# Kernel tuning notes

Hardware: AMD Instinct MI355X
Metric: run time of the kernel (lower is better)

## Reference

```python
import jax, jax.numpy as jnp
import numpy as np

N_WIRES = 9
N_QRAM_LAYERS = 3
N_QCLS_LAYERS = 5

X = jnp.array([[0, 1], [1, 0]], dtype=jnp.complex64)
CNOT = jnp.array([[1, 0, 0, 0], [0, 1, 0, 0], [0, 0, 0, 1], [0, 0, 1, 0]], dtype=jnp.complex64)


def _rx(t):
    c = jnp.cos(t / 2)
    s = jnp.sin(t / 2)
    # works for scalar t -> (2,2) or batched t [B] -> (B,2,2)
    return jnp.stack([jnp.stack([c + 0j, -1j * s], -1), jnp.stack([-1j * s, c + 0j], -1)], -2)


def _ry(t):
    c = jnp.cos(t / 2)
    s = jnp.sin(t / 2)
    return jnp.stack([jnp.stack([c, -s], -1), jnp.stack([s, c], -1)], -2).astype(jnp.complex64)


def _rz(t):
    e = jnp.exp(-0.5j * t)
    f = jnp.exp(0.5j * t)
    z = jnp.zeros_like(e)
    return jnp.stack([jnp.stack([e, z], -1), jnp.stack([z, f], -1)], -2)


def _rot(phi, theta, omega):
    # PennyLane Rot(phi, theta, omega) = RZ(omega) @ RY(theta) @ RZ(phi)
    return _rz(omega) @ _ry(theta) @ _rz(phi)


def _crz(t):
    e = jnp.exp(-0.5j * t)
    f = jnp.exp(0.5j * t)
    one = jnp.ones((), e.dtype)
    return jnp.diag(jnp.stack([one, one, e, f]))


def _crx(t):
    return jnp.eye(4, dtype=jnp.complex64).at[2:, 2:].set(_rx(t))


def apply_1q(state, U, w):
    # state: [B] + (2,)*N_WIRES ; wire w -> axis 1+w
    s = jnp.moveaxis(state, 1 + w, -1)
    if U.ndim == 3:  # per-sample gate (embedding)
        s = jnp.einsum('bij,b...j->b...i', U, s)
    else:
        s = jnp.einsum('ij,...j->...i', U, s)
    return jnp.moveaxis(s, -1, 1 + w)


def apply_2q(state, U, c, t):
    s = jnp.moveaxis(state, (1 + c, 1 + t), (-2, -1))
    shp = s.shape
    s = s.reshape(shp[:-2] + (4,))
    s = jnp.einsum('ij,...j->...i', U, s)
    return jnp.moveaxis(s.reshape(shp), (-2, -1), (1 + c, 1 + t))


def embed(state, adds):
    # AngleEmbedding: RX(adds[:, i]) on wire i
    for i in range(N_WIRES):
        state = apply_1q(state, _rx(adds[:, i]), i)
    return state


def entangle_block(state, p):
    # p: [36] = 4 params per wire-pair step
    j = 0
    for i in range(N_WIRES):
        ip = (i + 1) % N_WIRES
        state = apply_1q(state, _ry(p[j]), i)
        state = apply_1q(state, _ry(p[j + 1]), ip)
        state = apply_2q(state, CNOT, i, ip)
        state = apply_2q(state, _crz(p[j + 2]), i, ip)
        state = apply_1q(state, X, ip)
        state = apply_2q(state, _crx(p[j + 3]), i, ip)
        j += 4
    return state


def sel_layer(state, w, r):
    # one StronglyEntanglingLayers layer: Rot on each wire, then CNOT ring of range r
    for i in range(N_WIRES):
        state = apply_1q(state, _rot(w[i, 0], w[i, 1], w[i, 2]), i)
    for i in range(N_WIRES):
        state = apply_2q(state, CNOT, i, (i + r) % N_WIRES)
    return state


def circuit(adds, params, weights, params2):
    B = adds.shape[0]
    state = jnp.zeros((B,) + (2,) * N_WIRES, jnp.complex64)
    state = state.at[(slice(None),) + (0,) * N_WIRES].set(1.0)
    state = embed(state, adds)
    for l in range(N_QRAM_LAYERS):
        state = entangle_block(state, params[l * 36:(l + 1) * 36])
    for l in range(N_QRAM_LAYERS):
        r = (l % (N_WIRES - 1)) + 1  # PennyLane default ranges
        state = sel_layer(state, weights[l], r)
    for l in range(N_QCLS_LAYERS):
        state = entangle_block(state, params2[l * 36:(l + 1) * 36])
    probs = jnp.abs(state) ** 2
    p = probs.reshape(B, 2, -1).sum(-1)  # marginal over wire 0
    return p[:, 0] - p[:, 1]  # <PauliZ(0)>


def setup_inputs() -> dict:
    key = jax.random.key(0)
    k1, k2, k3, k4 = jax.random.split(key, 4)
    B = 8192
    return {
        'adds': jax.random.normal(k1, (B, N_WIRES), dtype=jnp.float32),
        'params': jax.random.normal(k2, (N_QRAM_LAYERS * 36,), dtype=jnp.float32),
        'weights': jax.random.normal(k3, (N_QRAM_LAYERS, N_WIRES, N_QRAM_LAYERS), dtype=jnp.float32),
        'params2': jax.random.normal(k4, (N_QCLS_LAYERS * 36,), dtype=jnp.float32),
    }


def reference(adds, params, weights, params2):
    return circuit(adds, params, weights, params2)
```

## Files before the change

kernel.cpp:

```cpp
#include <hip/hip_runtime.h>

#define NQ 9
#define NS 512
#define M2 1024

#define COEF_ROT_BASE (72*32)
#define COEF_FLOATS   (COEF_ROT_BASE + 27*8)

typedef __attribute__((ext_vector_type(8))) short bf16x8;
typedef __attribute__((ext_vector_type(4))) float f32x4;

__device__ inline unsigned short f2bf(float f){
  unsigned int u = __float_as_uint(f);
  u += 0x7fffu + ((u >> 16) & 1u);
  return (unsigned short)(u >> 16);
}


template<int LM>
__device__ inline float lxor(float v){
  if constexpr (LM == 1)
    return __int_as_float(__builtin_amdgcn_mov_dpp(__float_as_int(v), 0xB1, 0xF, 0xF, true));
  else if constexpr (LM == 2)
    return __int_as_float(__builtin_amdgcn_mov_dpp(__float_as_int(v), 0x4E, 0xF, 0xF, true));
  else if constexpr (LM == 3)
    return __int_as_float(__builtin_amdgcn_mov_dpp(__float_as_int(v), 0x1B, 0xF, 0xF, true));
  else if constexpr (LM < 32)
    return __int_as_float(__builtin_amdgcn_ds_swizzle(__float_as_int(v), (LM<<10)|0x1F));
  else
    return __shfl_xor(v, LM);
}

__device__ inline void apply_h(float& ax, float& ay, int p, const float* H,
                               float tx, float ty, float cx, float cy,
                               float bx, float by){
  const float* hx = H + p*4;
  const float* hy = H + 16 + p*4;
  float ox = ax, oy = ay;
  float nx = hx[0]*ox - hy[0]*oy + hx[1]*tx - hy[1]*ty
           + hx[2]*cx - hy[2]*cy + hx[3]*bx - hy[3]*by;
  float ny = hx[0]*oy + hy[0]*ox + hx[1]*ty + hy[1]*tx
           + hx[2]*cy + hy[2]*cx + hx[3]*by + hy[3]*bx;
  ax = nx; ay = ny;
}

template<int CM, int TM>
__device__ inline void step_lds(float& ax, float& ay, int i, float2* sh, const float* H){
  __syncthreads();
  sh[i] = make_float2(ax, ay);
  __syncthreads();
  float2 tv = sh[i ^ TM];
  float2 cv = sh[i ^ CM];
  float2 bv = sh[i ^ (CM ^ TM)];
  int p = ((i & CM) ? 2 : 0) | ((i & TM) ? 1 : 0);
  apply_h(ax, ay, p, H, tv.x, tv.y, cv.x, cv.y, bv.x, bv.y);
}

template<int CM, int TM>
__device__ inline void step_swz(float& ax, float& ay, int lane, const float* H){
  float tx = lxor<TM>(ax),      ty = lxor<TM>(ay);
  float cx = lxor<CM>(ax),      cy = lxor<CM>(ay);
  float bx = lxor<(CM^TM)>(ax), by = lxor<(CM^TM)>(ay);
  int p = ((lane & CM) ? 2 : 0) | ((lane & TM) ? 1 : 0);
  apply_h(ax, ay, p, H, tx, ty, cx, cy, bx, by);
}

template<int PM>
__device__ inline void rot_lds(float& ax, float& ay, int i, float2* sh, const float* U){
  __syncthreads();
  sh[i] = make_float2(ax, ay);
  __syncthreads();
  float2 pv = sh[i ^ PM];
  const float* u = U + (((i & PM) ? 1 : 0) << 2);
  float nx = u[0]*ax - u[1]*ay + u[2]*pv.x - u[3]*pv.y;
  float ny = u[0]*ay + u[1]*ax + u[2]*pv.y + u[3]*pv.x;
  ax = nx; ay = ny;
}

template<int LM>
__device__ inline void rot_swz(float& ax, float& ay, int lane, const float* U){
  float px = lxor<LM>(ax), py = lxor<LM>(ay);
  const float* u = U + (((lane & LM) ? 1 : 0) << 2);
  float nx = u[0]*ax - u[1]*ay + u[2]*px - u[3]*py;
  float ny = u[0]*ay + u[1]*ax + u[2]*py + u[3]*px;
  ax = nx; ay = ny;
}

__device__ inline void ring_rt(float& ax, float& ay, int i, float2* sh, int R){
  __syncthreads();
  sh[i] = make_float2(ax, ay);
  __syncthreads();
  int s = i;
  for (int k = 8; k >= 0; --k){
    int bc = 8 - k;
    int it = k + R; if (it >= 9) it -= 9;
    int bt = 8 - it;
    s ^= ((s >> bc) & 1) << bt;
  }
  float2 v = sh[s];
  ax = v.x; ay = v.y;
}


template<int I = 0>
__device__ inline void ent_blk(float& ax, float& ay, int i, int lane, float2* sh,
                               const float* Gbase){
  const float* H = Gbase + I*32;
  if constexpr      (I == 0) step_lds<0x100,0x080>(ax, ay, i, sh, H);
  else if constexpr (I == 1) step_lds<0x080,0x040>(ax, ay, i, sh, H);
  else if constexpr (I == 2) step_lds<0x040,0x020>(ax, ay, i, sh, H);
  else if constexpr (I == 3) step_swz<0x20,0x10>(ax, ay, lane, H);
  else if constexpr (I == 4) step_swz<0x10,0x08>(ax, ay, lane, H);
  else if constexpr (I == 5) step_swz<0x08,0x04>(ax, ay, lane, H);
  else if constexpr (I == 6) step_swz<0x04,0x02>(ax, ay, lane, H);
  else if constexpr (I == 7) step_swz<0x02,0x01>(ax, ay, lane, H);
  else                       step_lds<0x001,0x100>(ax, ay, i, sh, H);
  if constexpr (I < 8) ent_blk<I+1>(ax, ay, i, lane, sh, Gbase);
}

template<int I = 0>
__device__ inline void sel_rots_rt(float& ax, float& ay, int i, int lane, float2* sh,
                                   const float* ubase){
  const float* u = ubase + I*8;
  if constexpr      (I == 0) rot_lds<0x100>(ax, ay, i, sh, u);
  else if constexpr (I == 1) rot_lds<0x080>(ax, ay, i, sh, u);
  else if constexpr (I == 2) rot_lds<0x040>(ax, ay, i, sh, u);
  else if constexpr (I == 3) rot_swz<0x20>(ax, ay, lane, u);
  else if constexpr (I == 4) rot_swz<0x10>(ax, ay, lane, u);
  else if constexpr (I == 5) rot_swz<0x08>(ax, ay, lane, u);
  else if constexpr (I == 6) rot_swz<0x04>(ax, ay, lane, u);
  else if constexpr (I == 7) rot_swz<0x02>(ax, ay, lane, u);
  else                       rot_swz<0x01>(ax, ay, lane, u);
  if constexpr (I < 8) sel_rots_rt<I+1>(ax, ay, i, lane, sh, ubase);
}

__global__ __launch_bounds__(512) void sim_V(const float* __restrict__ params,
                                             const float* __restrict__ weights,
                                             const float* __restrict__ params2,
                                             unsigned short* __restrict__ A2){
  __shared__ float2 sh[512];
  __shared__ float scoef[COEF_FLOATS];
  int tid = threadIdx.x;

  if (tid < 72){
    int blk = tid / 9, I = tid % 9;
    const float* p = (blk < 3) ? params + blk*36 : params2 + (blk-3)*36;
    float s0,c0,s1,c1,s2,c2,s3,c3;
    __sincosf(0.5f*p[4*I+0], &s0, &c0);
    __sincosf(0.5f*p[4*I+1], &s1, &c1);
    __sincosf(0.5f*p[4*I+2], &s2, &c2);
    __sincosf(0.5f*p[4*I+3], &s3, &c3);
    float m[4][4] = {
      { c0*c1, -c0*s1, -s0*c1,  s0*s1},
      { c0*s1,  c0*c1, -s0*s1, -s0*c1},
      { s0*c1, -s0*s1,  c0*c1, -c0*s1},
      { s0*s1,  s0*c1,  c0*s1,  c0*c1}};
    float gx[4][4], gy[4][4];
    #pragma unroll
    for (int q = 0; q < 4; ++q){
      gx[0][q] = m[1][q];  gy[0][q] = 0.f;
      gx[1][q] = m[0][q];  gy[1][q] = 0.f;
      gx[2][q] =  c3*c2*m[2][q] - s3*s2*m[3][q];
      gy[2][q] =  c3*s2*m[2][q] - s3*c2*m[3][q];
      gx[3][q] =  s3*s2*m[2][q] + c3*c2*m[3][q];
      gy[3][q] = -(s3*c2*m[2][q] + c3*s2*m[3][q]);
    }
    float* dst = scoef + tid*32;
    #pragma unroll
    for (int pp = 0; pp < 4; ++pp)
      #pragma unroll
      for (int d = 0; d < 4; ++d){
        dst[pp*4+d]    = gx[pp][pp^d];
        dst[16+pp*4+d] = gy[pp][pp^d];
      }
  } else if (tid < 99){
    int r = tid - 72;
    int l = r / 9, i = r % 9;
    const float* w = weights + l*27 + 3*i;
    float phi = w[0], th = w[1], om = w[2];
    float sT,cT,sA,cA,sB,cB;
    __sincosf(0.5f*th, &sT, &cT);
    __sincosf(0.5f*(phi+om), &sA, &cA);
    __sincosf(0.5f*(om-phi), &sB, &cB);
    float* dst = scoef + COEF_ROT_BASE + r*8;
    dst[0] =  cA*cT;  dst[1] = -sA*cT;
    dst[2] = -cB*sT;  dst[3] =  sB*sT;
    dst[4] =  cA*cT;  dst[5] =  sA*cT;
    dst[6] =  cB*sT;  dst[7] =  sB*sT;
  }
  __syncthreads();

  int t = blockIdx.x;
  int i = tid;
  int lane = tid & 63;
  float ax, ay;
  int pc = __popc((unsigned)t) & 3;
  float prx = (pc==0) ? 1.f : (pc==2 ? -1.f : 0.f);
  float pry = (pc==3) ? 1.f : (pc==1 ? -1.f : 0.f);
  ax = (i == t) ? prx : 0.f;
  ay = (i == t) ? pry : 0.f;

  #pragma unroll 1
  for (int blk = 0; blk < 3; ++blk)
    ent_blk<0>(ax, ay, i, lane, sh, scoef + blk*288);
  #pragma unroll 1
  for (int L = 0; L < 3; ++L){
    sel_rots_rt<0>(ax, ay, i, lane, sh, scoef + COEF_ROT_BASE + L*72);
    ring_rt(ax, ay, i, sh, L + 1);
  }
  #pragma unroll 1
  for (int blk = 3; blk < 8; ++blk)
    ent_blk<0>(ax, ay, i, lane, sh, scoef + blk*288);

  A2[(size_t)i * NS + t]        = f2bf(ax);
  A2[(size_t)(i + NS) * NS + t] = f2bf(ay);
}

__global__ __launch_bounds__(256) void prep(const float* __restrict__ adds,
                                            unsigned short* __restrict__ cT,
                                            float* __restrict__ out, int B){
  int gid = blockIdx.x * 256 + threadIdx.x;
  int b = gid >> 6;
  int lane = gid & 63;
  if (b < B){
    const float* ab = adds + b * NQ;
    float cw[NQ], sw[NQ];
    #pragma unroll
    for (int w = 0; w < NQ; ++w)
      __sincosf(0.5f * ab[w], &sw[w], &cw[w]);
    float p6 = 1.f;
    #pragma unroll
    for (int w = 0; w < 6; ++w)
      p6 *= ((lane >> (5 - w)) & 1) ? sw[w] : cw[w];
    union { unsigned short u[8]; uint4 v; } pk;
    #pragma unroll
    for (int j = 0; j < 8; ++j){
      float p = p6 * (((j>>2)&1) ? sw[6] : cw[6])
                   * (((j>>1)&1) ? sw[7] : cw[7])
                   * (( j    &1) ? sw[8] : cw[8]);
      pk.u[j] = f2bf(p);
    }
    *(uint4*)(cT + (size_t)b * NS + lane*8) = pk.v;
  }
  if (gid < B) out[gid] = 0.f;
}

__global__ __launch_bounds__(256) void gemm_out(const unsigned short* __restrict__ A2,
                                                const unsigned short* __restrict__ cT,
                                                float* __restrict__ out){
  int bx = blockIdx.x;
  int by = blockIdx.y;
  int tid = threadIdx.x;
  int wave = tid >> 6, lane = tid & 63;
  int wy = wave >> 1, wx = wave & 1;
  int lane15 = lane & 15, quad = lane >> 4;
  int rowBase = by*128 + wy*64;
  int colBase = bx*128 + wx*64;
  const short* Ap = (const short*)A2;
  const short* Bp = (const short*)cT;

  f32x4 acc[4][4];
  #pragma unroll
  for (int i = 0; i < 4; ++i)
    #pragma unroll
    for (int j = 0; j < 4; ++j)
      acc[i][j] = (f32x4){0.f, 0.f, 0.f, 0.f};

  #pragma unroll 2
  for (int k0 = 0; k0 < NS; k0 += 32){
    bf16x8 a[4], b[4];
    #pragma unroll
    for (int mi = 0; mi < 4; ++mi)
      a[mi] = *(const bf16x8*)(Ap + (size_t)(rowBase + mi*16 + lane15)*NS + k0 + quad*8);
    #pragma unroll
    for (int ni = 0; ni < 4; ++ni)
      b[ni] = *(const bf16x8*)(Bp + (size_t)(colBase + ni*16 + lane15)*NS + k0 + quad*8);
    #pragma unroll
    for (int mi = 0; mi < 4; ++mi)
      #pragma unroll
      for (int ni = 0; ni < 4; ++ni)
        acc[mi][ni] = __builtin_amdgcn_mfma_f32_16x16x32_bf16(a[mi], b[ni], acc[mi][ni], 0, 0, 0);
  }

  float sign = (by & 2) ? -1.f : 1.f;
  #pragma unroll
  for (int ni = 0; ni < 4; ++ni){
    float cs = 0.f;
    #pragma unroll
    for (int mi = 0; mi < 4; ++mi)
      #pragma unroll
      for (int r = 0; r < 4; ++r)
        cs += acc[mi][ni][r] * acc[mi][ni][r];
    cs += __shfl_xor(cs, 16);
    cs += __shfl_xor(cs, 32);
    if (quad == 0)
      atomicAdd(out + colBase + ni*16 + lane15, sign * cs);
  }
}

extern "C" void kernel_launch(void* const* d_in, const int* in_sizes, int n_in,
                              void* d_out, int out_size, void* d_ws, size_t ws_size,
                              hipStream_t stream) {
  const float* adds    = (const float*)d_in[0];
  const float* params  = (const float*)d_in[1];
  const float* weights = (const float*)d_in[2];
  const float* params2 = (const float*)d_in[3];
  float* out = (float*)d_out;
  int B = in_sizes[0] / NQ;

  unsigned short* A2 = (unsigned short*)d_ws;
  unsigned short* cT = A2 + (size_t)M2 * NS;

  hipLaunchKernelGGL(sim_V, dim3(NS), dim3(512), 0, stream, params, weights, params2, A2);
  hipLaunchKernelGGL(prep, dim3((B * 64 + 255) / 256), dim3(256), 0, stream, adds, cT, out, B);
  hipLaunchKernelGGL(gemm_out, dim3(B / 128, 8), dim3(256), 0, stream, A2, cT, out);
}
```

Before: 119.9 us.

## Precompute gate coefficients once, fuse prep into sim kernel, factor in-wave gates

Gate coefficient computation moves out of each of the 512 sim blocks into a single-block precoef kernel that writes to workspace, so the per-block sincos work and its barrier go away. The prep (embedding) work is merged into the simulation kernel as extra blocks so the two run in one launch. In-wave entangling steps are rewritten as three sequential factored rotations using DPP/swizzle instead of a dense 4x4 complex matrix, which cuts arithmetic. Coefficients are now read from global memory rather than LDS, and the extra launch adds a dependency.

```diff
diff --git a/kernel.cpp b/kernel.cpp
--- a/kernel.cpp
+++ b/kernel.cpp
@@ -14,6 +14,68 @@
   unsigned int u = __float_as_uint(f);
   u += 0x7fffu + ((u >> 16) & 1u);
   return (unsigned short)(u >> 16);
+}
+
+__global__ __launch_bounds__(128) void precoef(const float* __restrict__ params,
+                                               const float* __restrict__ weights,
+                                               const float* __restrict__ params2,
+                                               float* __restrict__ coef){
+  int tid = threadIdx.x;
+  if (tid < 72){
+    int blk = tid / 9, I = tid % 9;
+    const float* p = (blk < 3) ? params + blk*36 : params2 + (blk-3)*36;
+    float s0,c0,s1,c1,s2,c2,s3,c3;
+    __sincosf(0.5f*p[4*I+0], &s0, &c0);
+    __sincosf(0.5f*p[4*I+1], &s1, &c1);
+    __sincosf(0.5f*p[4*I+2], &s2, &c2);
+    __sincosf(0.5f*p[4*I+3], &s3, &c3);
+    float* dst = coef + tid*32;
+    if (I == 0 || I == 1 || I == 2 || I == 8){
+      float m[4][4] = {
+        { c0*c1, -c0*s1, -s0*c1,  s0*s1},
+        { c0*s1,  c0*c1, -s0*s1, -s0*c1},
+        { s0*c1, -s0*s1,  c0*c1, -c0*s1},
+        { s0*s1,  s0*c1,  c0*s1,  c0*c1}};
+      float gx[4][4], gy[4][4];
+      #pragma unroll
+      for (int q = 0; q < 4; ++q){
+        gx[0][q] = m[1][q];  gy[0][q] = 0.f;
+        gx[1][q] = m[0][q];  gy[1][q] = 0.f;
+        gx[2][q] =  c3*c2*m[2][q] - s3*s2*m[3][q];
+        gy[2][q] =  c3*s2*m[2][q] - s3*c2*m[3][q];
+        gx[3][q] =  s3*s2*m[2][q] + c3*c2*m[3][q];
+        gy[3][q] = -(s3*c2*m[2][q] + c3*s2*m[3][q]);
+      }
+      #pragma unroll
+      for (int pp = 0; pp < 4; ++pp)
+        #pragma unroll
+        for (int d = 0; d < 4; ++d){
+          dst[pp*4+d]    = gx[pp][pp^d];
+          dst[16+pp*4+d] = gy[pp][pp^d];
+        }
+    } else {
+      dst[0] = c0;  dst[1] = s0;
+      dst[2] = c1;  dst[3] = s1;
+      dst[4] =  c3*c2;  dst[5] =  c3*s2;
+      dst[6] = -s3*s2;  dst[7] = -s3*c2;
+      #pragma unroll
+      for (int k = 8; k < 32; ++k) dst[k] = 0.f;
+    }
+  } else if (tid < 99){
+    int r = tid - 72;
+    int l = r / 9, i = r % 9;
+    const float* w = weights + l*27 + 3*i;
+    float phi = w[0], th = w[1], om = w[2];
+    float sT,cT,sA,cA,sB,cB;
+    __sincosf(0.5f*th, &sT, &cT);
+    __sincosf(0.5f*(phi+om), &sA, &cA);
+    __sincosf(0.5f*(om-phi), &sB, &cB);
+    float* dst = coef + COEF_ROT_BASE + r*8;
+    dst[0] =  cA*cT;  dst[1] = -sA*cT;
+    dst[2] = -cB*sT;  dst[3] =  sB*sT;
+    dst[4] =  cA*cT;  dst[5] =  sA*cT;
+    dst[6] =  cB*sT;  dst[7] =  sB*sT;
+  }
 }
 
 
@@ -31,58 +93,77 @@
     return __shfl_xor(v, LM);
 }
 
-__device__ inline void apply_h(float& ax, float& ay, int p, const float* H,
-                               float tx, float ty, float cx, float cy,
-                               float bx, float by){
-  const float* hx = H + p*4;
-  const float* hy = H + 16 + p*4;
-  float ox = ax, oy = ay;
-  float nx = hx[0]*ox - hy[0]*oy + hx[1]*tx - hy[1]*ty
-           + hx[2]*cx - hy[2]*cy + hx[3]*bx - hy[3]*by;
-  float ny = hx[0]*oy + hy[0]*ox + hx[1]*ty + hy[1]*tx
-           + hx[2]*cy + hy[2]*cx + hx[3]*by + hy[3]*bx;
-  ax = nx; ay = ny;
-}
-
 template<int CM, int TM>
-__device__ inline void step_lds(float& ax, float& ay, int i, float2* sh, const float* H){
+__device__ inline void step_h(float& ax, float& ay, int i, float2* sh,
+                              const float* __restrict__ g){
   __syncthreads();
   sh[i] = make_float2(ax, ay);
   __syncthreads();
   float2 tv = sh[i ^ TM];
   float2 cv = sh[i ^ CM];
   float2 bv = sh[i ^ (CM ^ TM)];
-  int p = ((i & CM) ? 2 : 0) | ((i & TM) ? 1 : 0);
-  apply_h(ax, ay, p, H, tv.x, tv.y, cv.x, cv.y, bv.x, bv.y);
+  bool cb = (i & CM) != 0, tb = (i & TM) != 0;
+  float hx[4], hy[4];
+  #pragma unroll
+  for (int d = 0; d < 4; ++d){
+    hx[d] = cb ? (tb ? g[12+d] : g[8+d]) : (tb ? g[4+d] : g[d]);
+    hy[d] = cb ? (tb ? g[28+d] : g[24+d]) : (tb ? g[20+d] : g[16+d]);
+  }
+  float ox = ax, oy = ay;
+  ax = hx[0]*ox - hy[0]*oy + hx[1]*tv.x - hy[1]*tv.y
+     + hx[2]*cv.x - hy[2]*cv.y + hx[3]*bv.x - hy[3]*bv.y;
+  ay = hx[0]*oy + hy[0]*ox + hx[1]*tv.y + hy[1]*tv.x
+     + hx[2]*cv.y + hy[2]*cv.x + hx[3]*bv.y + hy[3]*bv.x;
 }
 
 template<int CM, int TM>
-__device__ inline void step_swz(float& ax, float& ay, int lane, const float* H){
-  float tx = lxor<TM>(ax),      ty = lxor<TM>(ay);
-  float cx = lxor<CM>(ax),      cy = lxor<CM>(ay);
-  float bx = lxor<(CM^TM)>(ax), by = lxor<(CM^TM)>(ay);
-  int p = ((lane & CM) ? 2 : 0) | ((lane & TM) ? 1 : 0);
-  apply_h(ax, ay, p, H, tx, ty, cx, cy, bx, by);
+__device__ inline void step_3r(float& ax, float& ay, int lane,
+                               const float* __restrict__ g){
+  float c0=g[0], s0=g[1], c1=g[2], s1=g[3];
+  float Ax=g[4], Ay=g[5], Bx=g[6], By=g[7];
+  {
+    float px = lxor<CM>(ax), py = lxor<CM>(ay);
+    float se = (lane & CM) ? s0 : -s0;
+    ax = c0*ax + se*px;  ay = c0*ay + se*py;
+  }
+  {
+    float px = lxor<TM>(ax), py = lxor<TM>(ay);
+    float se = (lane & TM) ? s1 : -s1;
+    ax = c1*ax + se*px;  ay = c1*ay + se*py;
+  }
+  {
+    float px = lxor<TM>(ax), py = lxor<TM>(ay);
+    bool tb = (lane & TM) != 0;
+    float Ay2 = tb ? -Ay : Ay, Bx2 = tb ? -Bx : Bx;
+    float nx = Ax*ax - Ay2*ay + Bx2*px - By*py;
+    float ny = Ax*ay + Ay2*ax + Bx2*py + By*px;
+    bool cb = (lane & CM) != 0;
+    ax = cb ? nx : px;  ay = cb ? ny : py;
+  }
 }
 
 template<int PM>
-__device__ inline void rot_lds(float& ax, float& ay, int i, float2* sh, const float* U){
+__device__ inline void rot_img(float& ax, float& ay, int i, float2* sh,
+                               const float* __restrict__ u){
   __syncthreads();
   sh[i] = make_float2(ax, ay);
   __syncthreads();
   float2 pv = sh[i ^ PM];
-  const float* u = U + (((i & PM) ? 1 : 0) << 2);
-  float nx = u[0]*ax - u[1]*ay + u[2]*pv.x - u[3]*pv.y;
-  float ny = u[0]*ay + u[1]*ax + u[2]*pv.y + u[3]*pv.x;
+  bool hi = (i & PM) != 0;
+  float u0 = hi?u[4]:u[0], u1 = hi?u[5]:u[1], u2 = hi?u[6]:u[2], u3 = hi?u[7]:u[3];
+  float nx = u0*ax - u1*ay + u2*pv.x - u3*pv.y;
+  float ny = u0*ay + u1*ax + u2*pv.y + u3*pv.x;
   ax = nx; ay = ny;
 }
 
 template<int LM>
-__device__ inline void rot_swz(float& ax, float& ay, int lane, const float* U){
+__device__ inline void rot_swz(float& ax, float& ay, int lane,
+                               const float* __restrict__ u){
   float px = lxor<LM>(ax), py = lxor<LM>(ay);
-  const float* u = U + (((lane & LM) ? 1 : 0) << 2);
-  float nx = u[0]*ax - u[1]*ay + u[2]*px - u[3]*py;
-  float ny = u[0]*ay + u[1]*ax + u[2]*py + u[3]*px;
+  bool hi = (lane & LM) != 0;
+  float u0 = hi?u[4]:u[0], u1 = hi?u[5]:u[1], u2 = hi?u[6]:u[2], u3 = hi?u[7]:u[3];
+  float nx = u0*ax - u1*ay + u2*px - u3*py;
+  float ny = u0*ay + u1*ax + u2*py + u3*px;
   ax = nx; ay = ny;
 }
 
@@ -104,91 +185,62 @@
 
 template<int I = 0>
 __device__ inline void ent_blk(float& ax, float& ay, int i, int lane, float2* sh,
-                               const float* Gbase){
-  const float* H = Gbase + I*32;
-  if constexpr      (I == 0) step_lds<0x100,0x080>(ax, ay, i, sh, H);
-  else if constexpr (I == 1) step_lds<0x080,0x040>(ax, ay, i, sh, H);
-  else if constexpr (I == 2) step_lds<0x040,0x020>(ax, ay, i, sh, H);
-  else if constexpr (I == 3) step_swz<0x20,0x10>(ax, ay, lane, H);
-  else if constexpr (I == 4) step_swz<0x10,0x08>(ax, ay, lane, H);
-  else if constexpr (I == 5) step_swz<0x08,0x04>(ax, ay, lane, H);
-  else if constexpr (I == 6) step_swz<0x04,0x02>(ax, ay, lane, H);
-  else if constexpr (I == 7) step_swz<0x02,0x01>(ax, ay, lane, H);
-  else                       step_lds<0x001,0x100>(ax, ay, i, sh, H);
-  if constexpr (I < 8) ent_blk<I+1>(ax, ay, i, lane, sh, Gbase);
+                               const float* __restrict__ S){
+  const float* g = S + I*32;
+  if constexpr      (I == 0) step_h<0x100,0x080>(ax, ay, i, sh, g);
+  else if constexpr (I == 1) step_h<0x080,0x040>(ax, ay, i, sh, g);
+  else if constexpr (I == 2) step_h<0x040,0x020>(ax, ay, i, sh, g);
+  else if constexpr (I == 8) step_h<0x001,0x100>(ax, ay, i, sh, g);
+  else                       step_3r<(1<<(8-I)),(1<<(7-I))>(ax, ay, lane, g);
+  if constexpr (I < 8) ent_blk<I+1>(ax, ay, i, lane, sh, S);
 }
 
 template<int I = 0>
-__device__ inline void sel_rots_rt(float& ax, float& ay, int i, int lane, float2* sh,
-                                   const float* ubase){
-  const float* u = ubase + I*8;
-  if constexpr      (I == 0) rot_lds<0x100>(ax, ay, i, sh, u);
-  else if constexpr (I == 1) rot_lds<0x080>(ax, ay, i, sh, u);
-  else if constexpr (I == 2) rot_lds<0x040>(ax, ay, i, sh, u);
-  else if constexpr (I == 3) rot_swz<0x20>(ax, ay, lane, u);
-  else if constexpr (I == 4) rot_swz<0x10>(ax, ay, lane, u);
-  else if constexpr (I == 5) rot_swz<0x08>(ax, ay, lane, u);
-  else if constexpr (I == 6) rot_swz<0x04>(ax, ay, lane, u);
-  else if constexpr (I == 7) rot_swz<0x02>(ax, ay, lane, u);
-  else                       rot_swz<0x01>(ax, ay, lane, u);
-  if constexpr (I < 8) sel_rots_rt<I+1>(ax, ay, i, lane, sh, ubase);
-}
-
-__global__ __launch_bounds__(512) void sim_V(const float* __restrict__ params,
-                                             const float* __restrict__ weights,
-                                             const float* __restrict__ params2,
-                                             unsigned short* __restrict__ A2){
+__device__ inline void sel_rots(float& ax, float& ay, int i, int lane, float2* sh,
+                                const float* __restrict__ ub){
+  const float* u = ub + I*8;
+  if constexpr      (I == 0) rot_img<0x100>(ax, ay, i, sh, u);
+  else if constexpr (I == 1) rot_img<0x080>(ax, ay, i, sh, u);
+  else if constexpr (I == 2) rot_img<0x040>(ax, ay, i, sh, u);
+  else                       rot_swz<(1<<(8-I))>(ax, ay, lane, u);
+  if constexpr (I < 8) sel_rots<I+1>(ax, ay, i, lane, sh, ub);
+}
+
+__global__ __launch_bounds__(512) void sim_prep(const float* __restrict__ coef,
+                                                const float* __restrict__ adds,
+                                                unsigned short* __restrict__ A2,
+                                                unsigned short* __restrict__ cT,
+                                                float* __restrict__ out, int B){
   __shared__ float2 sh[512];
-  __shared__ float scoef[COEF_FLOATS];
   int tid = threadIdx.x;
 
-  if (tid < 72){
-    int blk = tid / 9, I = tid % 9;
-    const float* p = (blk < 3) ? params + blk*36 : params2 + (blk-3)*36;
-    float s0,c0,s1,c1,s2,c2,s3,c3;
-    __sincosf(0.5f*p[4*I+0], &s0, &c0);
-    __sincosf(0.5f*p[4*I+1], &s1, &c1);
-    __sincosf(0.5f*p[4*I+2], &s2, &c2);
-    __sincosf(0.5f*p[4*I+3], &s3, &c3);
-    float m[4][4] = {
-      { c0*c1, -c0*s1, -s0*c1,  s0*s1},
-      { c0*s1,  c0*c1, -s0*s1, -s0*c1},
-      { s0*c1, -s0*s1,  c0*c1, -c0*s1},
-      { s0*s1,  s0*c1,  c0*s1,  c0*c1}};
-    float gx[4][4], gy[4][4];
-    #pragma unroll
-    for (int q = 0; q < 4; ++q){
-      gx[0][q] = m[1][q];  gy[0][q] = 0.f;
-      gx[1][q] = m[0][q];  gy[1][q] = 0.f;
-      gx[2][q] =  c3*c2*m[2][q] - s3*s2*m[3][q];
-      gy[2][q] =  c3*s2*m[2][q] - s3*c2*m[3][q];
-      gx[3][q] =  s3*s2*m[2][q] + c3*c2*m[3][q];
-      gy[3][q] = -(s3*c2*m[2][q] + c3*s2*m[3][q]);
+  if (blockIdx.x >= NS){
+    int gid = (blockIdx.x - NS) * 512 + tid;
+    int b = gid >> 6;
+    int lane = gid & 63;
+    if (b < B){
+      const float* ab = adds + b * NQ;
+      float cw[NQ], sw[NQ];
+      #pragma unroll
+      for (int w = 0; w < NQ; ++w)
+        __sincosf(0.5f * ab[w], &sw[w], &cw[w]);
+      float p6 = 1.f;
+      #pragma unroll
+      for (int w = 0; w < 6; ++w)
+        p6 *= ((lane >> (5 - w)) & 1) ? sw[w] : cw[w];
+      union { unsigned short u[8]; uint4 v; } pk;
+      #pragma unroll
+      for (int j = 0; j < 8; ++j){
+        float p = p6 * (((j>>2)&1) ? sw[6] : cw[6])
+                     * (((j>>1)&1) ? sw[7] : cw[7])
+                     * (( j    &1) ? sw[8] : cw[8]);
+        pk.u[j] = f2bf(p);
+      }
+      *(uint4*)(cT + (size_t)b * NS + lane*8) = pk.v;
     }
-    float* dst = scoef + tid*32;
-    #pragma unroll
-    for (int pp = 0; pp < 4; ++pp)
-      #pragma unroll
-      for (int d = 0; d < 4; ++d){
-        dst[pp*4+d]    = gx[pp][pp^d];
-        dst[16+pp*4+d] = gy[pp][pp^d];
-      }
-  } else if (tid < 99){
-    int r = tid - 72;
-    int l = r / 9, i = r % 9;
-    const float* w = weights + l*27 + 3*i;
-    float phi = w[0], th = w[1], om = w[2];
-    float sT,cT,sA,cA,sB,cB;
-    __sincosf(0.5f*th, &sT, &cT);
-    __sincosf(0.5f*(phi+om), &sA, &cA);
-    __sincosf(0.5f*(om-phi), &sB, &cB);
-    float* dst = scoef + COEF_ROT_BASE + r*8;
-    dst[0] =  cA*cT;  dst[1] = -sA*cT;
-    dst[2] = -cB*sT;  dst[3] =  sB*sT;
-    dst[4] =  cA*cT;  dst[5] =  sA*cT;
-    dst[6] =  cB*sT;  dst[7] =  sB*sT;
-  }
-  __syncthreads();
+    if (gid < B) out[gid] = 0.f;
+    return;
+  }
 
   int t = blockIdx.x;
   int i = tid;
@@ -202,47 +254,18 @@
 
   #pragma unroll 1
   for (int blk = 0; blk < 3; ++blk)
-    ent_blk<0>(ax, ay, i, lane, sh, scoef + blk*288);
+    ent_blk<0>(ax, ay, i, lane, sh, coef + blk*288);
   #pragma unroll 1
   for (int L = 0; L < 3; ++L){
-    sel_rots_rt<0>(ax, ay, i, lane, sh, scoef + COEF_ROT_BASE + L*72);
+    sel_rots<0>(ax, ay, i, lane, sh, coef + COEF_ROT_BASE + L*72);
     ring_rt(ax, ay, i, sh, L + 1);
   }
   #pragma unroll 1
   for (int blk = 3; blk < 8; ++blk)
-    ent_blk<0>(ax, ay, i, lane, sh, scoef + blk*288);
+    ent_blk<0>(ax, ay, i, lane, sh, coef + blk*288);
 
   A2[(size_t)i * NS + t]        = f2bf(ax);
   A2[(size_t)(i + NS) * NS + t] = f2bf(ay);
-}
-
-__global__ __launch_bounds__(256) void prep(const float* __restrict__ adds,
-                                            unsigned short* __restrict__ cT,
-                                            float* __restrict__ out, int B){
-  int gid = blockIdx.x * 256 + threadIdx.x;
-  int b = gid >> 6;
-  int lane = gid & 63;
-  if (b < B){
-    const float* ab = adds + b * NQ;
-    float cw[NQ], sw[NQ];
-    #pragma unroll
-    for (int w = 0; w < NQ; ++w)
-      __sincosf(0.5f * ab[w], &sw[w], &cw[w]);
-    float p6 = 1.f;
-    #pragma unroll
-    for (int w = 0; w < 6; ++w)
-      p6 *= ((lane >> (5 - w)) & 1) ? sw[w] : cw[w];
-    union { unsigned short u[8]; uint4 v; } pk;
-    #pragma unroll
-    for (int j = 0; j < 8; ++j){
-      float p = p6 * (((j>>2)&1) ? sw[6] : cw[6])
-                   * (((j>>1)&1) ? sw[7] : cw[7])
-                   * (( j    &1) ? sw[8] : cw[8]);
-      pk.u[j] = f2bf(p);
-    }
-    *(uint4*)(cT + (size_t)b * NS + lane*8) = pk.v;
-  }
-  if (gid < B) out[gid] = 0.f;
 }
 
 __global__ __launch_bounds__(256) void gemm_out(const unsigned short* __restrict__ A2,
@@ -310,8 +333,11 @@
 
   unsigned short* A2 = (unsigned short*)d_ws;
   unsigned short* cT = A2 + (size_t)M2 * NS;
-
-  hipLaunchKernelGGL(sim_V, dim3(NS), dim3(512), 0, stream, params, weights, params2, A2);
-  hipLaunchKernelGGL(prep, dim3((B * 64 + 255) / 256), dim3(256), 0, stream, adds, cT, out, B);
+  float* coef = (float*)(cT + (size_t)B * NS);
+
+  int prepBlocks = (B * 64 + 511) / 512;
+  hipLaunchKernelGGL(precoef, dim3(1), dim3(128), 0, stream, params, weights, params2, coef);
+  hipLaunchKernelGGL(sim_prep, dim3(NS + prepBlocks), dim3(512), 0, stream,
+                     coef, adds, A2, cT, out, B);
   hipLaunchKernelGGL(gemm_out, dim3(B / 128, 8), dim3(256), 0, stream, A2, cT, out);
 }
```

Result: slower. 151.6 us (+26.4%).

## Fuse prep into sim kernel, double-buffer LDS steps, merge top-three-wire rotations

Applied to the files above, without the earlier changes.

Merges the prep kernel into the state-simulation kernel as extra blocks, which removes one launch and lets the two independent workloads run concurrently. LDS exchange steps now alternate between two buffers so each step needs one barrier instead of two. The three LDS-based single-qubit rotations on the top wires are folded into one 8x8 complex matrix applied in a single LDS pass, with the matrices precomputed per layer. Coefficient loads also become float4 reads. The cost is more shared memory and more arithmetic in the combined rotation pass.

```diff
diff --git a/kernel.cpp b/kernel.cpp
--- a/kernel.cpp
+++ b/kernel.cpp
@@ -5,7 +5,8 @@
 #define M2 1024
 
 #define COEF_ROT_BASE (72*32)
-#define COEF_FLOATS   (COEF_ROT_BASE + 27*8)
+#define COEF_R3_BASE  (COEF_ROT_BASE + 27*8)
+#define COEF_FLOATS   (COEF_R3_BASE + 3*128)
 
 typedef __attribute__((ext_vector_type(8))) short bf16x8;
 typedef __attribute__((ext_vector_type(4))) float f32x4;
@@ -31,64 +32,66 @@
     return __shfl_xor(v, LM);
 }
 
-__device__ inline void apply_h(float& ax, float& ay, int p, const float* H,
-                               float tx, float ty, float cx, float cy,
-                               float bx, float by){
-  const float* hx = H + p*4;
-  const float* hy = H + 16 + p*4;
+template<int CM, int TM>
+__device__ inline void step_h(float& ax, float& ay, int i, float2* buf,
+                              const float* g){
+  buf[i] = make_float2(ax, ay);
+  __syncthreads();
+  float2 tv = buf[i ^ TM];
+  float2 cv = buf[i ^ CM];
+  float2 bv = buf[i ^ (CM ^ TM)];
+  int p = ((i & CM) ? 2 : 0) | ((i & TM) ? 1 : 0);
+  float4 hx = *(const float4*)(g + p*4);
+  float4 hy = *(const float4*)(g + 16 + p*4);
   float ox = ax, oy = ay;
-  float nx = hx[0]*ox - hy[0]*oy + hx[1]*tx - hy[1]*ty
-           + hx[2]*cx - hy[2]*cy + hx[3]*bx - hy[3]*by;
-  float ny = hx[0]*oy + hy[0]*ox + hx[1]*ty + hy[1]*tx
-           + hx[2]*cy + hy[2]*cx + hx[3]*by + hy[3]*bx;
-  ax = nx; ay = ny;
+  ax = hx.x*ox - hy.x*oy + hx.y*tv.x - hy.y*tv.y
+     + hx.z*cv.x - hy.z*cv.y + hx.w*bv.x - hy.w*bv.y;
+  ay = hx.x*oy + hy.x*ox + hx.y*tv.y + hy.y*tv.x
+     + hx.z*cv.y + hy.z*cv.x + hx.w*bv.y + hy.w*bv.x;
 }
 
 template<int CM, int TM>
-__device__ inline void step_lds(float& ax, float& ay, int i, float2* sh, const float* H){
-  __syncthreads();
-  sh[i] = make_float2(ax, ay);
-  __syncthreads();
-  float2 tv = sh[i ^ TM];
-  float2 cv = sh[i ^ CM];
-  float2 bv = sh[i ^ (CM ^ TM)];
-  int p = ((i & CM) ? 2 : 0) | ((i & TM) ? 1 : 0);
-  apply_h(ax, ay, p, H, tv.x, tv.y, cv.x, cv.y, bv.x, bv.y);
-}
-
-template<int CM, int TM>
-__device__ inline void step_swz(float& ax, float& ay, int lane, const float* H){
+__device__ inline void step_swz(float& ax, float& ay, int lane, const float* g){
   float tx = lxor<TM>(ax),      ty = lxor<TM>(ay);
   float cx = lxor<CM>(ax),      cy = lxor<CM>(ay);
   float bx = lxor<(CM^TM)>(ax), by = lxor<(CM^TM)>(ay);
   int p = ((lane & CM) ? 2 : 0) | ((lane & TM) ? 1 : 0);
-  apply_h(ax, ay, p, H, tx, ty, cx, cy, bx, by);
-}
-
-template<int PM>
-__device__ inline void rot_lds(float& ax, float& ay, int i, float2* sh, const float* U){
+  float4 hx = *(const float4*)(g + p*4);
+  float4 hy = *(const float4*)(g + 16 + p*4);
+  float ox = ax, oy = ay;
+  ax = hx.x*ox - hy.x*oy + hx.y*tx - hy.y*ty
+     + hx.z*cx - hy.z*cy + hx.w*bx - hy.w*by;
+  ay = hx.x*oy + hy.x*ox + hx.y*ty + hy.y*tx
+     + hx.z*cy + hy.z*cx + hx.w*by + hy.w*bx;
+}
+
+__device__ inline void rot3_img(float& ax, float& ay, int i, float2* buf,
+                                const float* M){
+  buf[i] = make_float2(ax, ay);
   __syncthreads();
-  sh[i] = make_float2(ax, ay);
-  __syncthreads();
-  float2 pv = sh[i ^ PM];
-  const float* u = U + (((i & PM) ? 1 : 0) << 2);
-  float nx = u[0]*ax - u[1]*ay + u[2]*pv.x - u[3]*pv.y;
-  float ny = u[0]*ay + u[1]*ax + u[2]*pv.y + u[3]*pv.x;
+  int base = i & 63;
+  float nx = 0.f, ny = 0.f;
+  #pragma unroll
+  for (int q = 0; q < 8; ++q){
+    float2 v = buf[(q << 6) | base];
+    float mx = M[q*2], my = M[q*2+1];
+    nx += mx*v.x - my*v.y;
+    ny += mx*v.y + my*v.x;
+  }
   ax = nx; ay = ny;
 }
 
 template<int LM>
-__device__ inline void rot_swz(float& ax, float& ay, int lane, const float* U){
+__device__ inline void rot_swz(float& ax, float& ay, int lane, const float* u){
   float px = lxor<LM>(ax), py = lxor<LM>(ay);
-  const float* u = U + (((lane & LM) ? 1 : 0) << 2);
-  float nx = u[0]*ax - u[1]*ay + u[2]*px - u[3]*py;
-  float ny = u[0]*ay + u[1]*ax + u[2]*py + u[3]*px;
+  float4 uu = *(const float4*)(u + ((lane & LM) ? 4 : 0));
+  float nx = uu.x*ax - uu.y*ay + uu.z*px - uu.w*py;
+  float ny = uu.x*ay + uu.y*ax + uu.z*py + uu.w*px;
   ax = nx; ay = ny;
 }
 
-__device__ inline void ring_rt(float& ax, float& ay, int i, float2* sh, int R){
-  __syncthreads();
-  sh[i] = make_float2(ax, ay);
+__device__ inline void ring_rt(float& ax, float& ay, int i, float2* buf, int R){
+  buf[i] = make_float2(ax, ay);
   __syncthreads();
   int s = i;
   for (int k = 8; k >= 0; --k){
@@ -97,50 +100,70 @@
     int bt = 8 - it;
     s ^= ((s >> bc) & 1) << bt;
   }
-  float2 v = sh[s];
+  float2 v = buf[s];
   ax = v.x; ay = v.y;
 }
 
 
 template<int I = 0>
-__device__ inline void ent_blk(float& ax, float& ay, int i, int lane, float2* sh,
-                               const float* Gbase){
-  const float* H = Gbase + I*32;
-  if constexpr      (I == 0) step_lds<0x100,0x080>(ax, ay, i, sh, H);
-  else if constexpr (I == 1) step_lds<0x080,0x040>(ax, ay, i, sh, H);
-  else if constexpr (I == 2) step_lds<0x040,0x020>(ax, ay, i, sh, H);
-  else if constexpr (I == 3) step_swz<0x20,0x10>(ax, ay, lane, H);
-  else if constexpr (I == 4) step_swz<0x10,0x08>(ax, ay, lane, H);
-  else if constexpr (I == 5) step_swz<0x08,0x04>(ax, ay, lane, H);
-  else if constexpr (I == 6) step_swz<0x04,0x02>(ax, ay, lane, H);
-  else if constexpr (I == 7) step_swz<0x02,0x01>(ax, ay, lane, H);
-  else                       step_lds<0x001,0x100>(ax, ay, i, sh, H);
-  if constexpr (I < 8) ent_blk<I+1>(ax, ay, i, lane, sh, Gbase);
-}
-
-template<int I = 0>
-__device__ inline void sel_rots_rt(float& ax, float& ay, int i, int lane, float2* sh,
-                                   const float* ubase){
-  const float* u = ubase + I*8;
-  if constexpr      (I == 0) rot_lds<0x100>(ax, ay, i, sh, u);
-  else if constexpr (I == 1) rot_lds<0x080>(ax, ay, i, sh, u);
-  else if constexpr (I == 2) rot_lds<0x040>(ax, ay, i, sh, u);
-  else if constexpr (I == 3) rot_swz<0x20>(ax, ay, lane, u);
-  else if constexpr (I == 4) rot_swz<0x10>(ax, ay, lane, u);
-  else if constexpr (I == 5) rot_swz<0x08>(ax, ay, lane, u);
-  else if constexpr (I == 6) rot_swz<0x04>(ax, ay, lane, u);
-  else if constexpr (I == 7) rot_swz<0x02>(ax, ay, lane, u);
-  else                       rot_swz<0x01>(ax, ay, lane, u);
-  if constexpr (I < 8) sel_rots_rt<I+1>(ax, ay, i, lane, sh, ubase);
-}
-
-__global__ __launch_bounds__(512) void sim_V(const float* __restrict__ params,
-                                             const float* __restrict__ weights,
-                                             const float* __restrict__ params2,
-                                             unsigned short* __restrict__ A2){
-  __shared__ float2 sh[512];
+__device__ inline void ent_blk(float& ax, float& ay, int i, int lane,
+                               float2* bufA, float2* bufB, const float* S){
+  const float* g = S + I*32;
+  if constexpr      (I == 0) step_h<0x100,0x080>(ax, ay, i, bufA, g);
+  else if constexpr (I == 1) step_h<0x080,0x040>(ax, ay, i, bufB, g);
+  else if constexpr (I == 2) step_h<0x040,0x020>(ax, ay, i, bufA, g);
+  else if constexpr (I == 8) step_h<0x001,0x100>(ax, ay, i, bufB, g);
+  else                       step_swz<(1<<(8-I)),(1<<(7-I))>(ax, ay, lane, g);
+  if constexpr (I < 8) ent_blk<I+1>(ax, ay, i, lane, bufA, bufB, S);
+}
+
+template<int I = 3>
+__device__ inline void sel_lane_rots(float& ax, float& ay, int lane,
+                                     const float* ub){
+  rot_swz<(1<<(8-I))>(ax, ay, lane, ub + I*8);
+  if constexpr (I < 8) sel_lane_rots<I+1>(ax, ay, lane, ub);
+}
+
+__global__ __launch_bounds__(512) void sim_prep(const float* __restrict__ params,
+                                                const float* __restrict__ weights,
+                                                const float* __restrict__ params2,
+                                                const float* __restrict__ adds,
+                                                unsigned short* __restrict__ A2,
+                                                unsigned short* __restrict__ cT,
+                                                float* __restrict__ out, int B){
+  int tid = threadIdx.x;
+
+  if (blockIdx.x >= NS){
+    int gid = (blockIdx.x - NS) * 512 + tid;
+    int b = gid >> 6;
+    int lane = gid & 63;
+    if (b < B){
+      const float* ab = adds + b * NQ;
+      float cw[NQ], sw[NQ];
+      #pragma unroll
+      for (int w = 0; w < NQ; ++w)
+        __sincosf(0.5f * ab[w], &sw[w], &cw[w]);
+      float p6 = 1.f;
+      #pragma unroll
+      for (int w = 0; w < 6; ++w)
+        p6 *= ((lane >> (5 - w)) & 1) ? sw[w] : cw[w];
+      union { unsigned short u[8]; uint4 v; } pk;
+      #pragma unroll
+      for (int j = 0; j < 8; ++j){
+        float p = p6 * (((j>>2)&1) ? sw[6] : cw[6])
+                     * (((j>>1)&1) ? sw[7] : cw[7])
+                     * (( j    &1) ? sw[8] : cw[8]);
+        pk.u[j] = f2bf(p);
+      }
+      *(uint4*)(cT + (size_t)b * NS + lane*8) = pk.v;
+    }
+    if (gid < B) out[gid] = 0.f;
+    return;
+  }
+
+  __shared__ float2 bufA[512];
+  __shared__ float2 bufB[512];
   __shared__ float scoef[COEF_FLOATS];
-  int tid = threadIdx.x;
 
   if (tid < 72){
     int blk = tid / 9, I = tid % 9;
@@ -187,6 +210,38 @@
     dst[2] = -cB*sT;  dst[3] =  sB*sT;
     dst[4] =  cA*cT;  dst[5] =  sA*cT;
     dst[6] =  cB*sT;  dst[7] =  sB*sT;
+  } else if (tid < 123){
+    int idx = tid - 99;
+    int l = idx >> 3, p = idx & 7;
+    float e0x[3], e0y[3], e1x[3], e1y[3];
+    #pragma unroll
+    for (int w = 0; w < 3; ++w){
+      const float* wp = weights + l*27 + 3*w;
+      float phi = wp[0], th = wp[1], om = wp[2];
+      float sT,cT,sA,cA,sB,cB;
+      __sincosf(0.5f*th, &sT, &cT);
+      __sincosf(0.5f*(phi+om), &sA, &cA);
+      __sincosf(0.5f*(om-phi), &sB, &cB);
+      int pw = (p >> (2 - w)) & 1;
+      if (pw == 0){ e0x[w] =  cA*cT; e0y[w] = -sA*cT; e1x[w] = -cB*sT; e1y[w] =  sB*sT; }
+      else        { e0x[w] =  cB*sT; e0y[w] =  sB*sT; e1x[w] =  cA*cT; e1y[w] =  sA*cT; }
+    }
+    float* dst = scoef + COEF_R3_BASE + l*128 + p*16;
+    #pragma unroll
+    for (int q = 0; q < 8; ++q){
+      float rx = 1.f, ry = 0.f;
+      #pragma unroll
+      for (int w = 0; w < 3; ++w){
+        int qw = (q >> (2 - w)) & 1;
+        float fx = qw ? e1x[w] : e0x[w];
+        float fy = qw ? e1y[w] : e0y[w];
+        float nx = rx*fx - ry*fy;
+        float ny = rx*fy + ry*fx;
+        rx = nx; ry = ny;
+      }
+      dst[q*2]   = rx;
+      dst[q*2+1] = ry;
+    }
   }
   __syncthreads();
 
@@ -202,47 +257,19 @@
 
   #pragma unroll 1
   for (int blk = 0; blk < 3; ++blk)
-    ent_blk<0>(ax, ay, i, lane, sh, scoef + blk*288);
+    ent_blk<0>(ax, ay, i, lane, bufA, bufB, scoef + blk*288);
   #pragma unroll 1
   for (int L = 0; L < 3; ++L){
-    sel_rots_rt<0>(ax, ay, i, lane, sh, scoef + COEF_ROT_BASE + L*72);
-    ring_rt(ax, ay, i, sh, L + 1);
+    rot3_img(ax, ay, i, bufA, scoef + COEF_R3_BASE + L*128 + (i>>6)*16);
+    sel_lane_rots<3>(ax, ay, lane, scoef + COEF_ROT_BASE + L*72);
+    ring_rt(ax, ay, i, bufB, L + 1);
   }
   #pragma unroll 1
   for (int blk = 3; blk < 8; ++blk)
-    ent_blk<0>(ax, ay, i, lane, sh, scoef + blk*288);
+    ent_blk<0>(ax, ay, i, lane, bufA, bufB, scoef + blk*288);
 
   A2[(size_t)i * NS + t]        = f2bf(ax);
   A2[(size_t)(i + NS) * NS + t] = f2bf(ay);
-}
-
-__global__ __launch_bounds__(256) void prep(const float* __restrict__ adds,
-                                            unsigned short* __restrict__ cT,
-                                            float* __restrict__ out, int B){
-  int gid = blockIdx.x * 256 + threadIdx.x;
-  int b = gid >> 6;
-  int lane = gid & 63;
-  if (b < B){
-    const float* ab = adds + b * NQ;
-    float cw[NQ], sw[NQ];
-    #pragma unroll
-    for (int w = 0; w < NQ; ++w)
-      __sincosf(0.5f * ab[w], &sw[w], &cw[w]);
-    float p6 = 1.f;
-    #pragma unroll
-    for (int w = 0; w < 6; ++w)
-      p6 *= ((lane >> (5 - w)) & 1) ? sw[w] : cw[w];
-    union { unsigned short u[8]; uint4 v; } pk;
-    #pragma unroll
-    for (int j = 0; j < 8; ++j){
-      float p = p6 * (((j>>2)&1) ? sw[6] : cw[6])
-                   * (((j>>1)&1) ? sw[7] : cw[7])
-                   * (( j    &1) ? sw[8] : cw[8]);
-      pk.u[j] = f2bf(p);
-    }
-    *(uint4*)(cT + (size_t)b * NS + lane*8) = pk.v;
-  }
-  if (gid < B) out[gid] = 0.f;
 }
 
 __global__ __launch_bounds__(256) void gemm_out(const unsigned short* __restrict__ A2,
@@ -311,7 +338,8 @@
   unsigned short* A2 = (unsigned short*)d_ws;
   unsigned short* cT = A2 + (size_t)M2 * NS;
 
-  hipLaunchKernelGGL(sim_V, dim3(NS), dim3(512), 0, stream, params, weights, params2, A2);
-  hipLaunchKernelGGL(prep, dim3((B * 64 + 255) / 256), dim3(256), 0, stream, adds, cT, out, B);
+  int prepBlocks = (B * 64 + 511) / 512;
+  hipLaunchKernelGGL(sim_prep, dim3(NS + prepBlocks), dim3(512), 0, stream,
+                     params, weights, params2, adds, A2, cT, out, B);
   hipLaunchKernelGGL(gemm_out, dim3(B / 128, 8), dim3(256), 0, stream, A2, cT, out);
 }
```

Measured after the change: 118.3 us. About the same (-1.3%).
